# Kernel tuning notes

Hardware: AMD Instinct MI355X
Metric: run time of the kernel (lower is better)

Reference implementation:

```python
import jax, jax.numpy as jnp
import numpy as np

ALPHA = 0.1   # alpha_factor
BETA = 1.0    # beta_factor
NUM_CLASSES = 1000
B, D = 4096, 512


def setup_inputs() -> dict:
    key = jax.random.key(0)
    ks = jax.random.split(key, 7)
    return {
        "anchor": jax.random.normal(ks[0], (B, D), dtype=jnp.float32),
        "positive": jax.random.normal(ks[1], (B, D), dtype=jnp.float32),
        "negative": jax.random.normal(ks[2], (B, D), dtype=jnp.float32),
        "outputs": jax.random.normal(ks[3], (3 * B, NUM_CLASSES), dtype=jnp.float32),
        "labels_anchor": jax.random.randint(ks[4], (B,), 0, NUM_CLASSES, dtype=jnp.int32).astype(jnp.int64),
        "labels_neg": jax.random.randint(ks[5], (B,), 0, NUM_CLASSES, dtype=jnp.int32).astype(jnp.int64),
        "exemplars": jax.random.normal(ks[6], (NUM_CLASSES, D), dtype=jnp.float32),
    }


def reference(anchor, positive, negative, outputs, labels_anchor, labels_neg, exemplars):
    # cross-entropy (mean reduction) over concatenated labels [3B]
    labels = jnp.concatenate([labels_anchor, labels_anchor, labels_neg], axis=0)
    logp = jax.nn.log_softmax(outputs, axis=-1)                       # [3B, C]
    loss_softmax = -jnp.mean(jnp.take_along_axis(logp, labels[:, None], axis=1))

    # pairwise L2 distances anchor-to-exemplars via ||a||^2 + ||e||^2 - 2 a.e  -> [B, C]
    a_sq = jnp.sum(anchor * anchor, axis=1, keepdims=True)            # [B, 1]
    e_sq = jnp.sum(exemplars * exemplars, axis=1)[None, :]            # [1, C]
    d2 = a_sq + e_sq - 2.0 * (anchor @ exemplars.T)                   # [B, C]
    d_all = jnp.sqrt(jnp.maximum(d2, 0.0))

    d_ref = jnp.take_along_axis(d_all, labels_anchor[:, None], axis=1)[:, 0]  # [B]
    d_closest = jnp.min(d_all, axis=1)                                # [B]
    loss_center = jnp.sum(jax.nn.relu(d_ref - d_closest))

    tp = jnp.linalg.norm(anchor - positive, axis=1)                   # [B]
    tn = jnp.linalg.norm(anchor - negative, axis=1)                   # [B]
    loss_triplet = jnp.sum(jax.nn.relu(tp - tn))

    loss_total = loss_softmax + ALPHA * loss_center + BETA * loss_triplet
    return (loss_total, loss_triplet, loss_softmax, loss_center)
```

## Files before the change

### kernel.cpp

```cpp
#include <hip/hip_runtime.h>
#include <math.h>

#define BB 4096
#define DD 512
#define CC 1000

typedef __attribute__((ext_vector_type(8))) short short8;
typedef __attribute__((ext_vector_type(4))) float f32x4;

#define OFF_ABF  0
#define OFF_EBF  1048576
#define OFF_ESQ  1310720
#define OFF_ASQ  1311744
#define OFF_DREF 1315840
#define OFF_PMIN 1319936
#define OFF_CEP  1324032
#define OFF_TRP  1327104

__device__ __forceinline__ unsigned short f2bf(float x) {
    unsigned u = __float_as_uint(x);
    unsigned r = (u + 0x7FFFu + ((u >> 16) & 1u)) >> 16;
    return (unsigned short)r;
}

__global__ __launch_bounds__(512) void prep_kernel(
    const float* __restrict__ a, const float* __restrict__ p,
    const float* __restrict__ n, const float* __restrict__ ex,
    const int* __restrict__ la,
    unsigned short* __restrict__ Abf, unsigned short* __restrict__ Ebf,
    float* __restrict__ esq, float* __restrict__ asq,
    float* __restrict__ dref, float* __restrict__ tr_part,
    float* __restrict__ pmin)
{
    __shared__ float ps[8];
    const int bid = blockIdx.x;
    const int tid = threadIdx.x;
    const int w = tid >> 6, lane = tid & 63;

    if (bid < 512) {
        const int i = bid * 8 + w;
        const int label = la[i];
        const float4* ar = (const float4*)(a + (size_t)i * DD);
        const float4* pr = (const float4*)(p + (size_t)i * DD);
        const float4* nr = (const float4*)(n + (size_t)i * DD);
        const float4* er = (const float4*)(ex + (size_t)label * DD);
        float sa = 0.f, sp = 0.f, sn = 0.f, se = 0.f;
#pragma unroll
        for (int k = 0; k < 2; k++) {
            const int j = lane + k * 64;
            float4 av = ar[j], pv = pr[j], nv = nr[j], ev = er[j];
            union { unsigned short u[4]; uint2 q; } o;
            o.u[0]=f2bf(av.x); o.u[1]=f2bf(av.y); o.u[2]=f2bf(av.z); o.u[3]=f2bf(av.w);
            *(uint2*)(Abf + (size_t)i * DD + j * 4) = o.q;
            sa += av.x*av.x + av.y*av.y + av.z*av.z + av.w*av.w;
            float dx = av.x-pv.x, dy = av.y-pv.y, dz = av.z-pv.z, dw = av.w-pv.w;
            sp += dx*dx + dy*dy + dz*dz + dw*dw;
            dx = av.x-nv.x; dy = av.y-nv.y; dz = av.z-nv.z; dw = av.w-nv.w;
            sn += dx*dx + dy*dy + dz*dz + dw*dw;
            dx = av.x-ev.x; dy = av.y-ev.y; dz = av.z-ev.z; dw = av.w-ev.w;
            se += dx*dx + dy*dy + dz*dz + dw*dw;
        }
        for (int off = 32; off; off >>= 1) {
            sa += __shfl_xor(sa, off);
            sp += __shfl_xor(sp, off);
            sn += __shfl_xor(sn, off);
            se += __shfl_xor(se, off);
        }
        if (lane == 0) {
            asq[i]  = sa;
            dref[i] = sqrtf(se);
            pmin[i] = INFINITY;
            ps[w] = fmaxf(sqrtf(sp) - sqrtf(sn), 0.f);
        }
        __syncthreads();
        if (tid == 0) {
            float t = 0.f;
#pragma unroll
            for (int q = 0; q < 8; q++) t += ps[q];
            tr_part[bid] = t;
        }
    } else {
        const int c = (bid - 512) * 8 + w;
        float s = 0.f;
        if (c < CC) {
            const float4* row = (const float4*)(ex + (size_t)c * DD);
#pragma unroll
            for (int k = 0; k < 2; k++) {
                const int j = lane + k * 64;
                float4 v = row[j];
                union { unsigned short u[4]; uint2 q; } o;
                o.u[0]=f2bf(v.x); o.u[1]=f2bf(v.y); o.u[2]=f2bf(v.z); o.u[3]=f2bf(v.w);
                *(uint2*)(Ebf + (size_t)c * DD + j * 4) = o.q;
                s += v.x*v.x + v.y*v.y + v.z*v.z + v.w*v.w;
            }
            for (int off = 32; off; off >>= 1) s += __shfl_xor(s, off);
        } else {
            const uint2 z = make_uint2(0, 0);
#pragma unroll
            for (int k = 0; k < 2; k++) {
                const int j = lane + k * 64;
                *(uint2*)(Ebf + (size_t)c * DD + j * 4) = z;
            }
        }
        if (lane == 0) esq[c] = s;
    }
}

#define GL2LDS(gsrc, ldst) __builtin_amdgcn_global_load_lds( \
    (const __attribute__((address_space(1))) unsigned int*)(gsrc), \
    (__attribute__((address_space(3))) unsigned int*)(ldst), 16, 0, 0)

__global__ __launch_bounds__(512) void main_kernel(
    const unsigned short* __restrict__ Ab, const unsigned short* __restrict__ Eb,
    const float* __restrict__ asq, const float* __restrict__ esq,
    const float* __restrict__ outp,
    const int* __restrict__ la, const int* __restrict__ ln,
    float* __restrict__ pmin, float* __restrict__ ce_part)
{
    __shared__ unsigned short lA[2][128 * 64];
    __shared__ unsigned short lB[2][128 * 64];
    __shared__ float s_pm[4][128];
    __shared__ float ps[8];

    const int bid = blockIdx.x;
    const int tid = threadIdx.x;
    const int w = tid >> 6, lane = tid & 63;

    if (bid < 256) {
        const int strip = bid & 31, panel = bid >> 5;
        const int gm0 = strip * 128, gn0 = panel * 128;
        const int wm = w >> 2, wn = w & 3;
        const int hi = lane >> 4, lo = lane & 15;

        size_t srcA[2], srcB[2]; int dst2[2];
#pragma unroll
        for (int i = 0; i < 2; i++) {
            int c = tid + i * 512, r = c >> 3, s = c & 7;
            srcA[i] = ((size_t)(gm0 + r) << 9) + ((s ^ (r & 7)) << 3);
            srcB[i] = ((size_t)(gn0 + r) << 9) + ((s ^ (r & 7)) << 3);
            dst2[i] = c << 3;
        }

#define STAGE(buf, kt) do { \
        GL2LDS(Ab + srcA[0] + ((kt) << 6), &lA[buf][dst2[0]]); \
        GL2LDS(Ab + srcA[1] + ((kt) << 6), &lA[buf][dst2[1]]); \
        GL2LDS(Eb + srcB[0] + ((kt) << 6), &lB[buf][dst2[0]]); \
        GL2LDS(Eb + srcB[1] + ((kt) << 6), &lB[buf][dst2[1]]); \
    } while (0)

        f32x4 acc[4][2];
#pragma unroll
        for (int mi = 0; mi < 4; mi++)
#pragma unroll
            for (int ni = 0; ni < 2; ni++) acc[mi][ni] = (f32x4){0.f, 0.f, 0.f, 0.f};

        STAGE(0, 0);
        for (int kt = 0; kt < 8; kt++) {
            const int buf = kt & 1;
            if (kt < 7) {
                STAGE(buf ^ 1, kt + 1);
                asm volatile("s_waitcnt vmcnt(4)" ::: "memory");
            } else {
                asm volatile("s_waitcnt vmcnt(0)" ::: "memory");
            }
            __builtin_amdgcn_s_barrier();
            asm volatile("" ::: "memory");

#pragma unroll
            for (int kk = 0; kk < 2; kk++) {
                short8 af[4], bf[2];
#pragma unroll
                for (int mi = 0; mi < 4; mi++) {
                    int r = (wm << 6) + (mi << 4) + lo, s = (kk << 2) + hi;
                    af[mi] = *(const short8*)&lA[buf][(r << 6) + ((s ^ (r & 7)) << 3)];
                }
#pragma unroll
                for (int ni = 0; ni < 2; ni++) {
                    int r = (wn << 5) + (ni << 4) + lo, s = (kk << 2) + hi;
                    bf[ni] = *(const short8*)&lB[buf][(r << 6) + ((s ^ (r & 7)) << 3)];
                }
#pragma unroll
                for (int mi = 0; mi < 4; mi++)
#pragma unroll
                    for (int ni = 0; ni < 2; ni++)
                        acc[mi][ni] = __builtin_amdgcn_mfma_f32_16x16x32_bf16(af[mi], bf[ni], acc[mi][ni], 0, 0, 0);
            }
            asm volatile("" ::: "memory");
            __builtin_amdgcn_s_barrier();
        }
#undef STAGE

        float aq[4][4];
#pragma unroll
        for (int mi = 0; mi < 4; mi++) {
            float4 a0 = *(const float4*)&asq[gm0 + wm * 64 + mi * 16 + hi * 4];
            aq[mi][0]=a0.x; aq[mi][1]=a0.y; aq[mi][2]=a0.z; aq[mi][3]=a0.w;
        }
        float esqc[2]; int bad[2];
#pragma unroll
        for (int ni = 0; ni < 2; ni++) {
            int gn = gn0 + wn * 32 + ni * 16 + lo;
            esqc[ni] = esq[gn];
            bad[ni] = (gn >= CC);
        }
        float vmin[4][4];
#pragma unroll
        for (int mi = 0; mi < 4; mi++)
#pragma unroll
            for (int j = 0; j < 4; j++) {
                float best = INFINITY;
#pragma unroll
                for (int ni = 0; ni < 2; ni++) {
                    float d2 = aq[mi][j] + esqc[ni] - 2.f * acc[mi][ni][j];
                    float d = sqrtf(fmaxf(d2, 0.f));
                    if (bad[ni]) d = INFINITY;
                    best = fminf(best, d);
                }
                vmin[mi][j] = best;
            }
#pragma unroll
        for (int off = 1; off < 16; off <<= 1)
#pragma unroll
            for (int mi = 0; mi < 4; mi++)
#pragma unroll
                for (int j = 0; j < 4; j++)
                    vmin[mi][j] = fminf(vmin[mi][j], __shfl_xor(vmin[mi][j], off));

        if (lo == 0) {
#pragma unroll
            for (int mi = 0; mi < 4; mi++)
#pragma unroll
                for (int j = 0; j < 4; j++)
                    s_pm[wn][wm * 64 + mi * 16 + hi * 4 + j] = vmin[mi][j];
        }
        __syncthreads();
        if (tid < 128) {
            float m2 = fminf(fminf(s_pm[0][tid], s_pm[1][tid]),
                             fminf(s_pm[2][tid], s_pm[3][tid]));
            atomicMin((int*)pmin + gm0 + tid, __float_as_int(m2));
        }
    } else {
        const int cb = bid - 256;
        const int r = cb * 8 + w;
        const int label = (r < 2 * BB) ? la[r & (BB - 1)] : ln[r - 2 * BB];
        const float4* row4 = (const float4*)(outp + (size_t)r * CC);
        float4 v[4];
#pragma unroll
        for (int k = 0; k < 4; k++) {
            int j4 = lane + k * 64;
            v[k] = (j4 < 250) ? row4[j4]
                              : make_float4(-INFINITY, -INFINITY, -INFINITY, -INFINITY);
        }
        float m = -INFINITY;
#pragma unroll
        for (int k = 0; k < 4; k++)
            m = fmaxf(m, fmaxf(fmaxf(v[k].x, v[k].y), fmaxf(v[k].z, v[k].w)));
        for (int off = 32; off; off >>= 1) m = fmaxf(m, __shfl_xor(m, off));

        const int lj4 = label >> 2, lc = label & 3;
        float s = 0.f, lv = 0.f;
#pragma unroll
        for (int k = 0; k < 4; k++) {
            int j4 = lane + k * 64;
            s += __expf(v[k].x - m) + __expf(v[k].y - m)
               + __expf(v[k].z - m) + __expf(v[k].w - m);
            float comp = (lc == 0) ? v[k].x : (lc == 1) ? v[k].y : (lc == 2) ? v[k].z : v[k].w;
            lv += (j4 == lj4) ? comp : 0.f;
        }
        for (int off = 32; off; off >>= 1) {
            s += __shfl_xor(s, off);
            lv += __shfl_xor(lv, off);
        }
        if (lane == 0) ps[w] = -(lv - m - __logf(s));
        __syncthreads();
        if (tid == 0) {
            float t = 0.f;
#pragma unroll
            for (int q = 0; q < 8; q++) t += ps[q];
            ce_part[cb] = t;
        }
    }
}

__global__ __launch_bounds__(1024) void final_kernel(
    const float* __restrict__ ce_part, const float* __restrict__ tr_part,
    const float* __restrict__ pmin, const float* __restrict__ dref,
    float* __restrict__ out)
{
    int tid = threadIdx.x;
    float ce = 0.f, tr = (tid < 512) ? tr_part[tid] : 0.f, ctr = 0.f;
    if (tid < 1536) ce = ce_part[tid] + ((tid < 512) ? ce_part[tid + 1024] : 0.f);
#pragma unroll
    for (int a = 0; a < 4; a++) {
        int m = a * 1024 + tid;
        ctr += fmaxf(dref[m] - pmin[m], 0.f);
    }
    for (int off = 32; off; off >>= 1) {
        ce += __shfl_xor(ce, off);
        tr += __shfl_xor(tr, off);
        ctr += __shfl_xor(ctr, off);
    }
    __shared__ float s[3][16];
    int wid = tid >> 6, lane = tid & 63;
    if (lane == 0) { s[0][wid] = ce; s[1][wid] = tr; s[2][wid] = ctr; }
    __syncthreads();
    if (tid == 0) {
        float tce = 0.f, ttr = 0.f, tctr = 0.f;
#pragma unroll
        for (int w = 0; w < 16; w++) { tce += s[0][w]; ttr += s[1][w]; tctr += s[2][w]; }
        float lsm = tce / (3.f * BB);
        out[0] = lsm + 0.1f * tctr + 1.0f * ttr;
        out[1] = ttr;
        out[2] = lsm;
        out[3] = tctr;
    }
}

extern "C" void kernel_launch(void* const* d_in, const int* in_sizes, int n_in,
                              void* d_out, int out_size, void* d_ws, size_t ws_size,
                              hipStream_t stream) {
    const float* anchor   = (const float*)d_in[0];
    const float* positive = (const float*)d_in[1];
    const float* negative = (const float*)d_in[2];
    const float* outputs  = (const float*)d_in[3];
    const int*   la       = (const int*)d_in[4];
    const int*   ln       = (const int*)d_in[5];
    const float* ex       = (const float*)d_in[6];
    float* out = (float*)d_out;
    float* ws  = (float*)d_ws;

    unsigned short* Abf = (unsigned short*)(ws + OFF_ABF);
    unsigned short* Ebf = (unsigned short*)(ws + OFF_EBF);
    float* esq      = ws + OFF_ESQ;
    float* asq      = ws + OFF_ASQ;
    float* dref     = ws + OFF_DREF;
    float* pmin     = ws + OFF_PMIN;
    float* ce_part  = ws + OFF_CEP;
    float* tr_part  = ws + OFF_TRP;

    hipLaunchKernelGGL(prep_kernel,  dim3(640),  dim3(512),  0, stream,
                       anchor, positive, negative, ex, la, Abf, Ebf, esq, asq, dref, tr_part, pmin);
    hipLaunchKernelGGL(main_kernel,  dim3(1792), dim3(512),  0, stream,
                       Abf, Ebf, asq, esq, outputs, la, ln, pmin, ce_part);
    hipLaunchKernelGGL(final_kernel, dim3(1),    dim3(1024), 0, stream,
                       ce_part, tr_part, pmin, dref, out);
}
```

Measured before the change: 31.46 us.

## Move triplet work into main kernel, triple-buffer K=32 tiles, replace atomicMin with partials

Shrinks the prep kernel to only the bf16 conversion and squared norms. The triplet and reference-distance work (reading positive, negative and the label exemplar) moves into 512 extra blocks of the main kernel, where it can overlap with the GEMM and cross-entropy blocks. The GEMM now uses 32-wide K tiles with a three-stage LDS ring and a 4-way XOR swizzle. The atomicMin on per-row minima is replaced by per-panel partial writes that the final kernel reduces. The final kernel does more loads, and the smaller K tiles double the barrier count.

```diff
diff --git a/kernel.cpp b/kernel.cpp
--- a/kernel.cpp
+++ b/kernel.cpp
@@ -8,14 +8,14 @@
 typedef __attribute__((ext_vector_type(8))) short short8;
 typedef __attribute__((ext_vector_type(4))) float f32x4;
 
-#define OFF_ABF  0
-#define OFF_EBF  1048576
-#define OFF_ESQ  1310720
-#define OFF_ASQ  1311744
-#define OFF_DREF 1315840
-#define OFF_PMIN 1319936
-#define OFF_CEP  1324032
-#define OFF_TRP  1327104
+#define OFF_ABF   0
+#define OFF_EBF   1048576
+#define OFF_ESQ   1310720
+#define OFF_ASQ   1311744
+#define OFF_DREF  1315840
+#define OFF_PMINP 1319936
+#define OFF_CEP   1352704
+#define OFF_TRP   1354240
 
 __device__ __forceinline__ unsigned short f2bf(float x) {
     unsigned u = __float_as_uint(x);
@@ -24,61 +24,29 @@
 }
 
 __global__ __launch_bounds__(512) void prep_kernel(
-    const float* __restrict__ a, const float* __restrict__ p,
-    const float* __restrict__ n, const float* __restrict__ ex,
-    const int* __restrict__ la,
+    const float* __restrict__ a, const float* __restrict__ ex,
     unsigned short* __restrict__ Abf, unsigned short* __restrict__ Ebf,
-    float* __restrict__ esq, float* __restrict__ asq,
-    float* __restrict__ dref, float* __restrict__ tr_part,
-    float* __restrict__ pmin)
+    float* __restrict__ esq, float* __restrict__ asq)
 {
-    __shared__ float ps[8];
     const int bid = blockIdx.x;
     const int tid = threadIdx.x;
     const int w = tid >> 6, lane = tid & 63;
 
     if (bid < 512) {
         const int i = bid * 8 + w;
-        const int label = la[i];
         const float4* ar = (const float4*)(a + (size_t)i * DD);
-        const float4* pr = (const float4*)(p + (size_t)i * DD);
-        const float4* nr = (const float4*)(n + (size_t)i * DD);
-        const float4* er = (const float4*)(ex + (size_t)label * DD);
-        float sa = 0.f, sp = 0.f, sn = 0.f, se = 0.f;
+        float sa = 0.f;
 #pragma unroll
         for (int k = 0; k < 2; k++) {
             const int j = lane + k * 64;
-            float4 av = ar[j], pv = pr[j], nv = nr[j], ev = er[j];
+            float4 av = ar[j];
             union { unsigned short u[4]; uint2 q; } o;
             o.u[0]=f2bf(av.x); o.u[1]=f2bf(av.y); o.u[2]=f2bf(av.z); o.u[3]=f2bf(av.w);
             *(uint2*)(Abf + (size_t)i * DD + j * 4) = o.q;
             sa += av.x*av.x + av.y*av.y + av.z*av.z + av.w*av.w;
-            float dx = av.x-pv.x, dy = av.y-pv.y, dz = av.z-pv.z, dw = av.w-pv.w;
-            sp += dx*dx + dy*dy + dz*dz + dw*dw;
-            dx = av.x-nv.x; dy = av.y-nv.y; dz = av.z-nv.z; dw = av.w-nv.w;
-            sn += dx*dx + dy*dy + dz*dz + dw*dw;
-            dx = av.x-ev.x; dy = av.y-ev.y; dz = av.z-ev.z; dw = av.w-ev.w;
-            se += dx*dx + dy*dy + dz*dz + dw*dw;
-        }
-        for (int off = 32; off; off >>= 1) {
-            sa += __shfl_xor(sa, off);
-            sp += __shfl_xor(sp, off);
-            sn += __shfl_xor(sn, off);
-            se += __shfl_xor(se, off);
-        }
-        if (lane == 0) {
-            asq[i]  = sa;
-            dref[i] = sqrtf(se);
-            pmin[i] = INFINITY;
-            ps[w] = fmaxf(sqrtf(sp) - sqrtf(sn), 0.f);
-        }
-        __syncthreads();
-        if (tid == 0) {
-            float t = 0.f;
-#pragma unroll
-            for (int q = 0; q < 8; q++) t += ps[q];
-            tr_part[bid] = t;
-        }
+        }
+        for (int off = 32; off; off >>= 1) sa += __shfl_xor(sa, off);
+        if (lane == 0) asq[i] = sa;
     } else {
         const int c = (bid - 512) * 8 + w;
         float s = 0.f;
@@ -113,12 +81,15 @@
 __global__ __launch_bounds__(512) void main_kernel(
     const unsigned short* __restrict__ Ab, const unsigned short* __restrict__ Eb,
     const float* __restrict__ asq, const float* __restrict__ esq,
+    const float* __restrict__ a, const float* __restrict__ p,
+    const float* __restrict__ n, const float* __restrict__ ex,
     const float* __restrict__ outp,
     const int* __restrict__ la, const int* __restrict__ ln,
-    float* __restrict__ pmin, float* __restrict__ ce_part)
+    float* __restrict__ pminp, float* __restrict__ ce_part,
+    float* __restrict__ tr_part, float* __restrict__ dref)
 {
-    __shared__ unsigned short lA[2][128 * 64];
-    __shared__ unsigned short lB[2][128 * 64];
+    __shared__ unsigned short lA[3][128 * 32];
+    __shared__ unsigned short lB[3][128 * 32];
     __shared__ float s_pm[4][128];
     __shared__ float ps[8];
 
@@ -132,20 +103,15 @@
         const int wm = w >> 2, wn = w & 3;
         const int hi = lane >> 4, lo = lane & 15;
 
-        size_t srcA[2], srcB[2]; int dst2[2];
-#pragma unroll
-        for (int i = 0; i < 2; i++) {
-            int c = tid + i * 512, r = c >> 3, s = c & 7;
-            srcA[i] = ((size_t)(gm0 + r) << 9) + ((s ^ (r & 7)) << 3);
-            srcB[i] = ((size_t)(gn0 + r) << 9) + ((s ^ (r & 7)) << 3);
-            dst2[i] = c << 3;
-        }
+        const int r0 = tid >> 2, s0 = tid & 3;
+        const int g0 = s0 ^ (r0 & 3);
+        const size_t srcA = ((size_t)(gm0 + r0) << 9) + (g0 << 3);
+        const size_t srcB = ((size_t)(gn0 + r0) << 9) + (g0 << 3);
+        const int dst = tid << 3;
 
 #define STAGE(buf, kt) do { \
-        GL2LDS(Ab + srcA[0] + ((kt) << 6), &lA[buf][dst2[0]]); \
-        GL2LDS(Ab + srcA[1] + ((kt) << 6), &lA[buf][dst2[1]]); \
-        GL2LDS(Eb + srcB[0] + ((kt) << 6), &lB[buf][dst2[0]]); \
-        GL2LDS(Eb + srcB[1] + ((kt) << 6), &lB[buf][dst2[1]]); \
+        GL2LDS(Ab + srcA + ((kt) << 5), &lA[buf][dst]); \
+        GL2LDS(Eb + srcB + ((kt) << 5), &lB[buf][dst]); \
     } while (0)
 
         f32x4 acc[4][2];
@@ -155,36 +121,37 @@
             for (int ni = 0; ni < 2; ni++) acc[mi][ni] = (f32x4){0.f, 0.f, 0.f, 0.f};
 
         STAGE(0, 0);
-        for (int kt = 0; kt < 8; kt++) {
-            const int buf = kt & 1;
-            if (kt < 7) {
-                STAGE(buf ^ 1, kt + 1);
+        STAGE(1, 1);
+        for (int kt = 0; kt < 16; kt++) {
+            const int buf = kt % 3;
+            if (kt < 14) {
+                STAGE((kt + 2) % 3, kt + 2);
                 asm volatile("s_waitcnt vmcnt(4)" ::: "memory");
+            } else if (kt == 14) {
+                asm volatile("s_waitcnt vmcnt(2)" ::: "memory");
             } else {
                 asm volatile("s_waitcnt vmcnt(0)" ::: "memory");
             }
             __builtin_amdgcn_s_barrier();
             asm volatile("" ::: "memory");
 
-#pragma unroll
-            for (int kk = 0; kk < 2; kk++) {
-                short8 af[4], bf[2];
-#pragma unroll
-                for (int mi = 0; mi < 4; mi++) {
-                    int r = (wm << 6) + (mi << 4) + lo, s = (kk << 2) + hi;
-                    af[mi] = *(const short8*)&lA[buf][(r << 6) + ((s ^ (r & 7)) << 3)];
-                }
-#pragma unroll
-                for (int ni = 0; ni < 2; ni++) {
-                    int r = (wn << 5) + (ni << 4) + lo, s = (kk << 2) + hi;
-                    bf[ni] = *(const short8*)&lB[buf][(r << 6) + ((s ^ (r & 7)) << 3)];
-                }
-#pragma unroll
-                for (int mi = 0; mi < 4; mi++)
-#pragma unroll
-                    for (int ni = 0; ni < 2; ni++)
-                        acc[mi][ni] = __builtin_amdgcn_mfma_f32_16x16x32_bf16(af[mi], bf[ni], acc[mi][ni], 0, 0, 0);
-            }
+            short8 af[4], bf[2];
+#pragma unroll
+            for (int mi = 0; mi < 4; mi++) {
+                int r = (wm << 6) + (mi << 4) + lo;
+                af[mi] = *(const short8*)&lA[buf][(r << 5) + ((hi ^ (r & 3)) << 3)];
+            }
+#pragma unroll
+            for (int ni = 0; ni < 2; ni++) {
+                int r = (wn << 5) + (ni << 4) + lo;
+                bf[ni] = *(const short8*)&lB[buf][(r << 5) + ((hi ^ (r & 3)) << 3)];
+            }
+#pragma unroll
+            for (int mi = 0; mi < 4; mi++)
+#pragma unroll
+                for (int ni = 0; ni < 2; ni++)
+                    acc[mi][ni] = __builtin_amdgcn_mfma_f32_16x16x32_bf16(af[mi], bf[ni], acc[mi][ni], 0, 0, 0);
+
             asm volatile("" ::: "memory");
             __builtin_amdgcn_s_barrier();
         }
@@ -237,9 +204,9 @@
         if (tid < 128) {
             float m2 = fminf(fminf(s_pm[0][tid], s_pm[1][tid]),
                              fminf(s_pm[2][tid], s_pm[3][tid]));
-            atomicMin((int*)pmin + gm0 + tid, __float_as_int(m2));
-        }
-    } else {
+            pminp[((size_t)(gm0 + tid) << 3) + panel] = m2;
+        }
+    } else if (bid < 1792) {
         const int cb = bid - 256;
         const int r = cb * 8 + w;
         const int label = (r < 2 * BB) ? la[r & (BB - 1)] : ln[r - 2 * BB];
@@ -279,21 +246,63 @@
             for (int q = 0; q < 8; q++) t += ps[q];
             ce_part[cb] = t;
         }
+    } else {
+        const int i = (bid - 1792) * 8 + w;
+        const int label = la[i];
+        const float4* ar = (const float4*)(a + (size_t)i * DD);
+        const float4* pr = (const float4*)(p + (size_t)i * DD);
+        const float4* nr = (const float4*)(n + (size_t)i * DD);
+        const float4* er = (const float4*)(ex + (size_t)label * DD);
+        float sp = 0.f, sn = 0.f, se = 0.f;
+#pragma unroll
+        for (int k = 0; k < 2; k++) {
+            const int j = lane + k * 64;
+            float4 av = ar[j], pv = pr[j], nv = nr[j], ev = er[j];
+            float dx = av.x-pv.x, dy = av.y-pv.y, dz = av.z-pv.z, dw = av.w-pv.w;
+            sp += dx*dx + dy*dy + dz*dz + dw*dw;
+            dx = av.x-nv.x; dy = av.y-nv.y; dz = av.z-nv.z; dw = av.w-nv.w;
+            sn += dx*dx + dy*dy + dz*dz + dw*dw;
+            dx = av.x-ev.x; dy = av.y-ev.y; dz = av.z-ev.z; dw = av.w-ev.w;
+            se += dx*dx + dy*dy + dz*dz + dw*dw;
+        }
+        for (int off = 32; off; off >>= 1) {
+            sp += __shfl_xor(sp, off);
+            sn += __shfl_xor(sn, off);
+            se += __shfl_xor(se, off);
+        }
+        if (lane == 0) {
+            dref[i] = sqrtf(se);
+            ps[w] = fmaxf(sqrtf(sp) - sqrtf(sn), 0.f);
+        }
+        __syncthreads();
+        if (tid == 0) {
+            float t = 0.f;
+#pragma unroll
+            for (int q = 0; q < 8; q++) t += ps[q];
+            tr_part[bid - 1792] = t;
+        }
     }
 }
 
 __global__ __launch_bounds__(1024) void final_kernel(
     const float* __restrict__ ce_part, const float* __restrict__ tr_part,
-    const float* __restrict__ pmin, const float* __restrict__ dref,
+    const float* __restrict__ pminp, const float* __restrict__ dref,
     float* __restrict__ out)
 {
     int tid = threadIdx.x;
-    float ce = 0.f, tr = (tid < 512) ? tr_part[tid] : 0.f, ctr = 0.f;
-    if (tid < 1536) ce = ce_part[tid] + ((tid < 512) ? ce_part[tid + 1024] : 0.f);
-#pragma unroll
-    for (int a = 0; a < 4; a++) {
-        int m = a * 1024 + tid;
-        ctr += fmaxf(dref[m] - pmin[m], 0.f);
+    float ce = ce_part[tid] + ((tid < 512) ? ce_part[tid + 1024] : 0.f);
+    float tr = (tid < 512) ? tr_part[tid] : 0.f;
+    float ctr = 0.f;
+    float4 d4 = *(const float4*)&dref[tid * 4];
+#pragma unroll
+    for (int k = 0; k < 4; k++) {
+        int m = tid * 4 + k;
+        float4 p0 = *(const float4*)&pminp[(size_t)m * 8];
+        float4 p1 = *(const float4*)&pminp[(size_t)m * 8 + 4];
+        float mn = fminf(fminf(fminf(p0.x, p0.y), fminf(p0.z, p0.w)),
+                         fminf(fminf(p1.x, p1.y), fminf(p1.z, p1.w)));
+        float dr = (k == 0) ? d4.x : (k == 1) ? d4.y : (k == 2) ? d4.z : d4.w;
+        ctr += fmaxf(dr - mn, 0.f);
     }
     for (int off = 32; off; off >>= 1) {
         ce += __shfl_xor(ce, off);
@@ -307,7 +316,7 @@
     if (tid == 0) {
         float tce = 0.f, ttr = 0.f, tctr = 0.f;
 #pragma unroll
-        for (int w = 0; w < 16; w++) { tce += s[0][w]; ttr += s[1][w]; tctr += s[2][w]; }
+        for (int q = 0; q < 16; q++) { tce += s[0][q]; ttr += s[1][q]; tctr += s[2][q]; }
         float lsm = tce / (3.f * BB);
         out[0] = lsm + 0.1f * tctr + 1.0f * ttr;
         out[1] = ttr;
@@ -334,14 +343,15 @@
     float* esq      = ws + OFF_ESQ;
     float* asq      = ws + OFF_ASQ;
     float* dref     = ws + OFF_DREF;
-    float* pmin     = ws + OFF_PMIN;
+    float* pminp    = ws + OFF_PMINP;
     float* ce_part  = ws + OFF_CEP;
     float* tr_part  = ws + OFF_TRP;
 
     hipLaunchKernelGGL(prep_kernel,  dim3(640),  dim3(512),  0, stream,
-                       anchor, positive, negative, ex, la, Abf, Ebf, esq, asq, dref, tr_part, pmin);
-    hipLaunchKernelGGL(main_kernel,  dim3(1792), dim3(512),  0, stream,
-                       Abf, Ebf, asq, esq, outputs, la, ln, pmin, ce_part);
+                       anchor, ex, Abf, Ebf, esq, asq);
+    hipLaunchKernelGGL(main_kernel,  dim3(2304), dim3(512),  0, stream,
+                       Abf, Ebf, asq, esq, anchor, positive, negative, ex,
+                       outputs, la, ln, pminp, ce_part, tr_part, dref);
     hipLaunchKernelGGL(final_kernel, dim3(1),    dim3(1024), 0, stream,
-                       ce_part, tr_part, pmin, dref, out);
-}
+                       ce_part, tr_part, pminp, dref, out);
+}
```

New measurement: 32.98 us. 4.9% more time.
